# Kernel tuning notes

Hardware: AMD Instinct MI355X
Metric: run time of the kernel (lower is better)

Reference implementation:

```python
import jax, jax.numpy as jnp
import numpy as np

HIDDEN = 1024
HEADS = 16
B, L = 2, 2048


def _xavier(key, shape):
    fan_in, fan_out = shape[1], shape[0]
    limit = float(np.sqrt(6.0 / (fan_in + fan_out)))
    return jax.random.uniform(key, shape, jnp.float32, -limit, limit)


def setup_inputs() -> dict:
    key = jax.random.key(0)
    ks = jax.random.split(key, 6)
    return {
        "query": jax.random.normal(ks[0], (B, L, HIDDEN), jnp.float32),
        "bias": jax.random.normal(ks[1], (B, 1, 1, L), jnp.float32),
        "Wq": _xavier(ks[2], (HIDDEN, HIDDEN)), "bq": jnp.zeros((HIDDEN,), jnp.float32),
        "Wk": _xavier(ks[3], (HIDDEN, HIDDEN)), "bk": jnp.zeros((HIDDEN,), jnp.float32),
        "Wv": _xavier(ks[4], (HIDDEN, HIDDEN)), "bv": jnp.zeros((HIDDEN,), jnp.float32),
        "Wo": _xavier(ks[5], (HIDDEN, HIDDEN)), "bo": jnp.zeros((HIDDEN,), jnp.float32),
    }


def _split_heads(x):
    b, l, c = x.shape
    return x.reshape(b, l, HEADS, c // HEADS).transpose(0, 2, 1, 3)  # [B,H,L,d]


def reference(query, bias, Wq, bq, Wk, bk, Wv, bv, Wo, bo):
    d_head = HIDDEN // HEADS
    q = query @ Wq.T + bq
    k = query @ Wk.T + bk
    v = query @ Wv.T + bv
    q = _split_heads(q) * (d_head ** -0.5)  # [B,H,L,d]
    k = _split_heads(k)
    v = _split_heads(v)
    logits = jnp.einsum("bhqd,bhkd->bhqk", q, k) + bias  # [B,H,L,L]
    weights = jax.nn.softmax(logits, axis=-1)
    x = jnp.einsum("bhqk,bhkd->bhqd", weights, v)  # [B,H,L,d]
    x = x.transpose(0, 2, 1, 3).reshape(query.shape[0], query.shape[1], HIDDEN)
    return x @ Wo.T + bo
```

## Files before the change

### kernel.cpp

```cpp
#include <hip/hip_runtime.h>
#include <hip/hip_fp16.h>
#include <stdint.h>

#define HIDDEN 1024
#define HEADS  16
#define DH     64
#define B_     2
#define L_     2048
#define M_TOT  (B_ * L_)
#define ELEMS  (M_TOT * HIDDEN)
#define LOG2E  1.44269504088896340736f

typedef _Float16 f16;
typedef _Float16 f16x4 __attribute__((ext_vector_type(4)));
typedef _Float16 f16x8 __attribute__((ext_vector_type(8)));
typedef float    f32x4 __attribute__((ext_vector_type(4)));
typedef uint32_t u32;
typedef __attribute__((address_space(1))) u32 gu32;
typedef __attribute__((address_space(3))) u32 su32;

#define MFMA16(a, b, c) __builtin_amdgcn_mfma_f32_16x16x16f16(a, b, c, 0, 0, 0)
#define MFMA32(a, b, c) __builtin_amdgcn_mfma_f32_16x16x32_f16(a, b, c, 0, 0, 0)


__global__ __launch_bounds__(256)
void convert_f16(const float* __restrict__ query,
                 const float* __restrict__ Wq, const float* __restrict__ Wk,
                 const float* __restrict__ Wv, const float* __restrict__ Wo,
                 f16* __restrict__ Qh, f16* __restrict__ Wh)
{
    const int NQ4 = ELEMS / 4;
    const int NW4 = (HIDDEN * HIDDEN) / 4;
    const int total = NQ4 + 4 * NW4;
    for (int u = blockIdx.x * 256 + threadIdx.x; u < total; u += gridDim.x * 256) {
        float4 v; f16* dp;
        if (u < NQ4) {
            v = ((const float4*)query)[u];
            dp = Qh + (size_t)u * 4;
        } else {
            const int u2 = u - NQ4;
            const int w = u2 >> 18;
            const int off = u2 & (NW4 - 1);
            const float* W = (w == 0) ? Wq : (w == 1) ? Wk : (w == 2) ? Wv : Wo;
            v = ((const float4*)W)[off];
            dp = Wh + (size_t)u2 * 4;
        }
        f16x4 h = { (f16)v.x, (f16)v.y, (f16)v.z, (f16)v.w };
        *(f16x4*)dp = h;
    }
}

template<int TM, int TN>
__device__ __forceinline__
void gemm_loop(const f16* __restrict__ A, const f16* __restrict__ W,
               int mb, int nb, f32x4 (&acc)[TM / 32][TN / 32])
{
    __shared__ f16 As[2][TM * 32];
    __shared__ f16 Bs[2][TN * 32];

    const int tid  = threadIdx.x;
    const int lane = tid & 63;
    const int wave = tid >> 6;
    const int quad = lane >> 4;
    const int l16  = lane & 15;
    const int wm   = (wave >> 1) * (TM / 2);
    const int wn   = (wave & 1) * (TN / 2);

    constexpr int AISS = TM / 64;
    constexpr int BISS = TN / 64;
    int aoff[AISS], boff[BISS];
#pragma unroll
    for (int q = 0; q < AISS; q++) {
        const int p16 = (wave * AISS + q) * 64 + lane;
        const int r = p16 >> 2;
        const int c8 = (p16 & 3) ^ ((r >> 1) & 3);
        aoff[q] = (mb + r) * HIDDEN + c8 * 8;
    }
#pragma unroll
    for (int q = 0; q < BISS; q++) {
        const int p16 = (wave * BISS + q) * 64 + lane;
        const int r = p16 >> 2;
        const int c8 = (p16 & 3) ^ ((r >> 1) & 3);
        boff[q] = (nb + r) * HIDDEN + c8 * 8;
    }

#pragma unroll
    for (int q = 0; q < AISS; q++)
        __builtin_amdgcn_global_load_lds((gu32*)&A[aoff[q]],
                                         (su32*)&As[0][(wave * AISS + q) * 512], 16, 0, 0);
#pragma unroll
    for (int q = 0; q < BISS; q++)
        __builtin_amdgcn_global_load_lds((gu32*)&W[boff[q]],
                                         (su32*)&Bs[0][(wave * BISS + q) * 512], 16, 0, 0);
    __syncthreads();

    for (int kb = 0; kb < HIDDEN; kb += 32) {
        const int buf = (kb >> 5) & 1;
        const int nkb = (kb + 32 < HIDDEN) ? kb + 32 : 0;

#pragma unroll
        for (int q = 0; q < AISS; q++)
            __builtin_amdgcn_global_load_lds((gu32*)&A[aoff[q] + nkb],
                                             (su32*)&As[buf ^ 1][(wave * AISS + q) * 512], 16, 0, 0);
#pragma unroll
        for (int q = 0; q < BISS; q++)
            __builtin_amdgcn_global_load_lds((gu32*)&W[boff[q] + nkb],
                                             (su32*)&Bs[buf ^ 1][(wave * BISS + q) * 512], 16, 0, 0);

        f16x8 af[TM / 32], bf[TN / 32];
#pragma unroll
        for (int i = 0; i < TM / 32; i++) {
            const int r = wm + i * 16 + l16;
            af[i] = *(const f16x8*)&As[buf][r * 32 + (quad ^ ((r >> 1) & 3)) * 8];
        }
#pragma unroll
        for (int j = 0; j < TN / 32; j++) {
            const int r = wn + j * 16 + l16;
            bf[j] = *(const f16x8*)&Bs[buf][r * 32 + (quad ^ ((r >> 1) & 3)) * 8];
        }
#pragma unroll
        for (int i = 0; i < TM / 32; i++)
#pragma unroll
            for (int j = 0; j < TN / 32; j++)
                acc[i][j] = MFMA32(af[i], bf[j], acc[i][j]);
        __syncthreads();
    }
}

__global__ __launch_bounds__(256)
void proj_qkv(const f16* __restrict__ A, const f16* __restrict__ W,
              const float* __restrict__ bq, const float* __restrict__ bk,
              const float* __restrict__ bv,
              f16* __restrict__ Qo, f16* __restrict__ Ko, f16* __restrict__ Vo)
{
    f32x4 acc[4][4] = {};
    const int mb = blockIdx.x * 128, nb = blockIdx.y * 128;
    gemm_loop<128, 128>(A, W, mb, nb, acc);

    const int lane = threadIdx.x & 63, wave = threadIdx.x >> 6;
    const int quad = lane >> 4, l16 = lane & 15;
    const int wm = (wave >> 1) * 64, wn = (wave & 1) * 64;
    const int nsel = nb >> 10;
    const int nbase = nb & 1023;

    if (nsel < 2) {
        const float* bias = nsel ? bk : bq;
        f16* out = nsel ? Ko : Qo;
        const float scale = nsel ? 1.0f : 0.125f * LOG2E;
#pragma unroll
        for (int i = 0; i < 4; i++)
#pragma unroll
            for (int j = 0; j < 4; j++) {
                const int n1 = nbase + wn + j * 16 + l16;
                const float bn = bias[n1];
                const int h = n1 >> 6, dd = n1 & 63;
#pragma unroll
                for (int r = 0; r < 4; r++) {
                    const int m = mb + wm + i * 16 + quad * 4 + r;
                    const int b = m >> 11, l = m & (L_ - 1);
                    out[(((b * HEADS + h) * L_) + l) * DH + dd] =
                        (f16)((acc[i][j][r] + bn) * scale);
                }
            }
    } else {
#pragma unroll
        for (int i = 0; i < 4; i++)
#pragma unroll
            for (int j = 0; j < 4; j++) {
                const int n1 = nbase + wn + j * 16 + l16;
                const float bn = bv[n1];
                const int h = n1 >> 6, dd = n1 & 63;
                const int m0 = mb + wm + i * 16 + quad * 4;
                const int b = m0 >> 11, l0 = m0 & (L_ - 1);
                f16x4 pk;
#pragma unroll
                for (int r = 0; r < 4; r++) pk[r] = (f16)(acc[i][j][r] + bn);
                *(f16x4*)&Vo[((size_t)(b * HEADS + h) * DH + dd) * L_ + l0] = pk;
            }
    }
}

__global__ __launch_bounds__(256)
void proj_out(const f16* __restrict__ A, const f16* __restrict__ W,
              const float* __restrict__ bo, float* __restrict__ out)
{
    f32x4 acc[4][2] = {};
    const int mb = blockIdx.x * 128, nb = blockIdx.y * 64;
    gemm_loop<128, 64>(A, W, mb, nb, acc);

    const int lane = threadIdx.x & 63, wave = threadIdx.x >> 6;
    const int quad = lane >> 4, l16 = lane & 15;
    const int wm = (wave >> 1) * 64, wn = (wave & 1) * 32;
#pragma unroll
    for (int i = 0; i < 4; i++)
#pragma unroll
        for (int j = 0; j < 2; j++) {
            const int n = nb + wn + j * 16 + l16;
            const float bn = bo[n];
#pragma unroll
            for (int r = 0; r < 4; r++) {
                const int m = mb + wm + i * 16 + quad * 4 + r;
                out[m * HIDDEN + n] = acc[i][j][r] + bn;
            }
        }
}

__global__ __launch_bounds__(256)
void attn(const f16* __restrict__ Q, const f16* __restrict__ K,
          const f16* __restrict__ Vt, const float* __restrict__ bias,
          f16* __restrict__ X)
{
    __shared__ f16 Ks[2][64 * 64];
    __shared__ f16 Vs[2][64 * 64];
    __shared__ float biasl[L_];

    const int tid  = threadIdx.x;
    const int lane = tid & 63;
    const int wave = tid >> 6;
    const int quad = lane >> 4;
    const int l16  = lane & 15;

    const int bh = blockIdx.x >> 4;
    const int b  = bh >> 4, h = bh & 15;
    const int qrow0 = (blockIdx.x & 15) * 128 + wave * 32;

    const f16* Qh  = Q  + (size_t)bh * L_ * DH;
    const f16* Kh  = K  + (size_t)bh * L_ * DH;
    const f16* Vth = Vt + (size_t)bh * DH * L_;

    {
        const float4* bb = (const float4*)(bias + b * L_);
        for (int i = tid; i < L_ / 4; i += 256) {
            const float4 v = bb[i];
            biasl[i * 4 + 0] = v.x * LOG2E;
            biasl[i * 4 + 1] = v.y * LOG2E;
            biasl[i * 4 + 2] = v.z * LOG2E;
            biasl[i * 4 + 3] = v.w * LOG2E;
        }
    }

    int krow[2], kcol[2];
#pragma unroll
    for (int q = 0; q < 2; q++) {
        const int grp = wave * 2 + q;
        const int r = grp * 8 + (lane >> 3);
        const int u = (lane & 7) ^ (r & 7);
        krow[q] = r; kcol[q] = u * 8;
    }

    f16x8 qf[2][2];
#pragma unroll
    for (int qt = 0; qt < 2; qt++)
#pragma unroll
        for (int hh = 0; hh < 2; hh++)
            qf[qt][hh] = *(const f16x8*)&Qh[(qrow0 + qt * 16 + l16) * DH + hh * 32 + quad * 8];

#pragma unroll
    for (int q = 0; q < 2; q++) {
        __builtin_amdgcn_global_load_lds((gu32*)(Kh + (size_t)krow[q] * DH + kcol[q]),
                                         (su32*)&Ks[0][(wave * 2 + q) * 512], 16, 0, 0);
        __builtin_amdgcn_global_load_lds((gu32*)(Vth + (size_t)krow[q] * L_ + kcol[q]),
                                         (su32*)&Vs[0][(wave * 2 + q) * 512], 16, 0, 0);
    }

    f32x4 o[2][4] = {};
    f32x4 osum[2] = {};
    const f16x4 ones = { (f16)1.f, (f16)1.f, (f16)1.f, (f16)1.f };
    __syncthreads();

#pragma unroll 1
    for (int kb = 0; kb < L_; kb += 64) {
        const int buf = (kb >> 6) & 1;
        const int nkb = (kb + 64 < L_) ? kb + 64 : 0;

#pragma unroll
        for (int q = 0; q < 2; q++) {
            __builtin_amdgcn_global_load_lds(
                (gu32*)(Kh + (size_t)(nkb + krow[q]) * DH + kcol[q]),
                (su32*)&Ks[buf ^ 1][(wave * 2 + q) * 512], 16, 0, 0);
            __builtin_amdgcn_global_load_lds(
                (gu32*)(Vth + (size_t)krow[q] * L_ + nkb + kcol[q]),
                (su32*)&Vs[buf ^ 1][(wave * 2 + q) * 512], 16, 0, 0);
        }

#pragma unroll
        for (int c = 0; c < 4; c++) {
            const int krowc = c * 16 + l16;
            const f16x8 ka0 = *(const f16x8*)&Ks[buf][krowc * 64 + (quad ^ (krowc & 7)) * 8];
            const f16x8 ka1 = *(const f16x8*)&Ks[buf][krowc * 64 + ((quad + 4) ^ (krowc & 7)) * 8];
            f16x4 va[4];
#pragma unroll
            for (int t = 0; t < 4; t++) {
                const int vr = t * 16 + l16;
                const int uu = (c * 2 + (quad >> 1)) ^ (vr & 7);
                va[t] = *(const f16x4*)&Vs[buf][vr * 64 + uu * 8 + (quad & 1) * 4];
            }
            const f32x4 blv = *(const f32x4*)&biasl[kb + c * 16 + quad * 4];

#pragma unroll
            for (int qt = 0; qt < 2; qt++) {
                f32x4 z = blv;
                z = MFMA32(ka0, qf[qt][0], z);
                z = MFMA32(ka1, qf[qt][1], z);
                const f16x4 pb = { (f16)__builtin_amdgcn_exp2f(z[0]),
                                   (f16)__builtin_amdgcn_exp2f(z[1]),
                                   (f16)__builtin_amdgcn_exp2f(z[2]),
                                   (f16)__builtin_amdgcn_exp2f(z[3]) };
#pragma unroll
                for (int t = 0; t < 4; t++)
                    o[qt][t] = MFMA16(va[t], pb, o[qt][t]);
                osum[qt] = MFMA16(ones, pb, osum[qt]);
            }
        }
        __syncthreads();
    }

#pragma unroll
    for (int qt = 0; qt < 2; qt++) {
        const float inv = 1.0f / osum[qt][0];
        const size_t qrow = (size_t)b * L_ + qrow0 + qt * 16 + l16;
#pragma unroll
        for (int t = 0; t < 4; t++) {
            f16x4 pk;
#pragma unroll
            for (int r = 0; r < 4; r++) pk[r] = (f16)(o[qt][t][r] * inv);
            *(f16x4*)&X[qrow * HIDDEN + h * DH + t * 16 + quad * 4] = pk;
        }
    }
}

extern "C" void kernel_launch(void* const* d_in, const int* in_sizes, int n_in,
                              void* d_out, int out_size, void* d_ws, size_t ws_size,
                              hipStream_t stream)
{
    const float* query = (const float*)d_in[0];
    const float* bias  = (const float*)d_in[1];
    const float* Wq = (const float*)d_in[2]; const float* bq = (const float*)d_in[3];
    const float* Wk = (const float*)d_in[4]; const float* bk = (const float*)d_in[5];
    const float* Wv = (const float*)d_in[6]; const float* bv = (const float*)d_in[7];
    const float* Wo = (const float*)d_in[8]; const float* bo = (const float*)d_in[9];
    float* out = (float*)d_out;

    f16* Wh = (f16*)d_ws;
    f16* Qh = Wh + 4096 * 1024;
    f16* Kf = Qh + ELEMS;
    f16* Vf = Kf + ELEMS;
    f16* Qf = Vf + ELEMS;
    f16* Xf = Qh;

    convert_f16<<<2048, 256, 0, stream>>>(query, Wq, Wk, Wv, Wo, Qh, Wh);
    proj_qkv<<<dim3(32, 24), 256, 0, stream>>>(Qh, Wh, bq, bk, bv, Qf, Kf, Vf);
    attn<<<512, 256, 0, stream>>>(Qf, Kf, Vf, bias, Xf);
    proj_out<<<dim3(32, 16), 256, 0, stream>>>(Xf, Wh + 3072 * 1024, bo, out);
}
```

Measured before the change: 208.6 us.

## Use 16x16x32 MFMA for PV product with permuted K rows and block swizzle

```diff
diff --git a/kernel.cpp b/kernel.cpp
--- a/kernel.cpp
+++ b/kernel.cpp
@@ -19,7 +19,6 @@
 typedef __attribute__((address_space(1))) u32 gu32;
 typedef __attribute__((address_space(3))) u32 su32;
 
-#define MFMA16(a, b, c) __builtin_amdgcn_mfma_f32_16x16x16f16(a, b, c, 0, 0, 0)
 #define MFMA32(a, b, c) __builtin_amdgcn_mfma_f32_16x16x32_f16(a, b, c, 0, 0, 0)
 
 
@@ -220,9 +219,11 @@
     const int quad = lane >> 4;
     const int l16  = lane & 15;
 
-    const int bh = blockIdx.x >> 4;
+    const int bid = (int)blockIdx.x;
+    const int lb  = (bid & 7) * 64 + (bid >> 3);
+    const int bh = lb >> 4;
     const int b  = bh >> 4, h = bh & 15;
-    const int qrow0 = (blockIdx.x & 15) * 128 + wave * 32;
+    const int qrow0 = (lb & 15) * 128 + wave * 32;
 
     const f16* Qh  = Q  + (size_t)bh * L_ * DH;
     const f16* Kh  = K  + (size_t)bh * L_ * DH;
@@ -239,13 +240,15 @@
         }
     }
 
-    int krow[2], kcol[2];
+    int krow[2], kcol[2], vcol[2];
 #pragma unroll
     for (int q = 0; q < 2; q++) {
-        const int grp = wave * 2 + q;
-        const int r = grp * 8 + (lane >> 3);
-        const int u = (lane & 7) ^ (r & 7);
-        krow[q] = r; kcol[q] = u * 8;
+        const int p = (wave * 2 + q) * 64 + lane;
+        const int r = p >> 3;
+        const int w = p & 7;
+        krow[q] = r;
+        kcol[q] = (w ^ (r & 7) ^ (((r >> 3) & 1) << 2)) * 8;
+        vcol[q] = (w ^ (r & 7)) * 8;
     }
 
     f16x8 qf[2][2];
@@ -254,18 +257,38 @@
 #pragma unroll
         for (int hh = 0; hh < 2; hh++)
             qf[qt][hh] = *(const f16x8*)&Qh[(qrow0 + qt * 16 + l16) * DH + hh * 32 + quad * 8];
+
+    int koffX[2][2], koffY[2][2], voff[2][4];
+#pragma unroll
+    for (int g = 0; g < 2; g++) {
+        const int rX = g * 32 + ((l16 >> 2) << 3) + (l16 & 3);
+        const int rY = rX + 4;
+        const int gkX = (rX & 7) ^ (((rX >> 3) & 1) << 2);
+        const int gkY = (rY & 7) ^ (((rY >> 3) & 1) << 2);
+#pragma unroll
+        for (int hh = 0; hh < 2; hh++) {
+            koffX[g][hh] = rX * 64 + (((hh * 4 + quad) ^ gkX) << 3);
+            koffY[g][hh] = rY * 64 + (((hh * 4 + quad) ^ gkY) << 3);
+        }
+#pragma unroll
+        for (int t = 0; t < 4; t++) {
+            const int vr = t * 16 + l16;
+            voff[g][t] = vr * 64 + (((g * 4 + quad) ^ (vr & 7)) << 3);
+        }
+    }
 
 #pragma unroll
     for (int q = 0; q < 2; q++) {
         __builtin_amdgcn_global_load_lds((gu32*)(Kh + (size_t)krow[q] * DH + kcol[q]),
                                          (su32*)&Ks[0][(wave * 2 + q) * 512], 16, 0, 0);
-        __builtin_amdgcn_global_load_lds((gu32*)(Vth + (size_t)krow[q] * L_ + kcol[q]),
+        __builtin_amdgcn_global_load_lds((gu32*)(Vth + (size_t)krow[q] * L_ + vcol[q]),
                                          (su32*)&Vs[0][(wave * 2 + q) * 512], 16, 0, 0);
     }
 
     f32x4 o[2][4] = {};
     f32x4 osum[2] = {};
-    const f16x4 ones = { (f16)1.f, (f16)1.f, (f16)1.f, (f16)1.f };
+    const f16x8 ones8 = { (f16)1.f, (f16)1.f, (f16)1.f, (f16)1.f,
+                          (f16)1.f, (f16)1.f, (f16)1.f, (f16)1.f };
     __syncthreads();
 
 #pragma unroll 1
@@ -279,37 +302,39 @@
                 (gu32*)(Kh + (size_t)(nkb + krow[q]) * DH + kcol[q]),
                 (su32*)&Ks[buf ^ 1][(wave * 2 + q) * 512], 16, 0, 0);
             __builtin_amdgcn_global_load_lds(
-                (gu32*)(Vth + (size_t)krow[q] * L_ + nkb + kcol[q]),
+                (gu32*)(Vth + (size_t)krow[q] * L_ + nkb + vcol[q]),
                 (su32*)&Vs[buf ^ 1][(wave * 2 + q) * 512], 16, 0, 0);
         }
 
 #pragma unroll
-        for (int c = 0; c < 4; c++) {
-            const int krowc = c * 16 + l16;
-            const f16x8 ka0 = *(const f16x8*)&Ks[buf][krowc * 64 + (quad ^ (krowc & 7)) * 8];
-            const f16x8 ka1 = *(const f16x8*)&Ks[buf][krowc * 64 + ((quad + 4) ^ (krowc & 7)) * 8];
-            f16x4 va[4];
-#pragma unroll
-            for (int t = 0; t < 4; t++) {
-                const int vr = t * 16 + l16;
-                const int uu = (c * 2 + (quad >> 1)) ^ (vr & 7);
-                va[t] = *(const f16x4*)&Vs[buf][vr * 64 + uu * 8 + (quad & 1) * 4];
-            }
-            const f32x4 blv = *(const f32x4*)&biasl[kb + c * 16 + quad * 4];
+        for (int g = 0; g < 2; g++) {
+            const f16x8 kx0 = *(const f16x8*)&Ks[buf][koffX[g][0]];
+            const f16x8 kx1 = *(const f16x8*)&Ks[buf][koffX[g][1]];
+            const f16x8 ky0 = *(const f16x8*)&Ks[buf][koffY[g][0]];
+            const f16x8 ky1 = *(const f16x8*)&Ks[buf][koffY[g][1]];
+            f16x8 va[4];
+#pragma unroll
+            for (int t = 0; t < 4; t++)
+                va[t] = *(const f16x8*)&Vs[buf][voff[g][t]];
+            const f32x4 blvX = *(const f32x4*)&biasl[kb + g * 32 + quad * 8];
+            const f32x4 blvY = *(const f32x4*)&biasl[kb + g * 32 + quad * 8 + 4];
 
 #pragma unroll
             for (int qt = 0; qt < 2; qt++) {
-                f32x4 z = blv;
-                z = MFMA32(ka0, qf[qt][0], z);
-                z = MFMA32(ka1, qf[qt][1], z);
-                const f16x4 pb = { (f16)__builtin_amdgcn_exp2f(z[0]),
-                                   (f16)__builtin_amdgcn_exp2f(z[1]),
-                                   (f16)__builtin_amdgcn_exp2f(z[2]),
-                                   (f16)__builtin_amdgcn_exp2f(z[3]) };
+                f32x4 zx = blvX, zy = blvY;
+                zx = MFMA32(kx0, qf[qt][0], zx);
+                zx = MFMA32(kx1, qf[qt][1], zx);
+                zy = MFMA32(ky0, qf[qt][0], zy);
+                zy = MFMA32(ky1, qf[qt][1], zy);
+                const f16x8 pb = {
+                    (f16)__builtin_amdgcn_exp2f(zx[0]), (f16)__builtin_amdgcn_exp2f(zx[1]),
+                    (f16)__builtin_amdgcn_exp2f(zx[2]), (f16)__builtin_amdgcn_exp2f(zx[3]),
+                    (f16)__builtin_amdgcn_exp2f(zy[0]), (f16)__builtin_amdgcn_exp2f(zy[1]),
+                    (f16)__builtin_amdgcn_exp2f(zy[2]), (f16)__builtin_amdgcn_exp2f(zy[3]) };
 #pragma unroll
                 for (int t = 0; t < 4; t++)
-                    o[qt][t] = MFMA16(va[t], pb, o[qt][t]);
-                osum[qt] = MFMA16(ones, pb, osum[qt]);
+                    o[qt][t] = MFMA32(va[t], pb, o[qt][t]);
+                osum[qt] = MFMA32(ones8, pb, osum[qt]);
             }
         }
         __syncthreads();
```

Result: faster. 202.7 us (-2.8%).
